# Performance work log

Measured on AMD Instinct MI355X. Metric: run time of the kernel, lower is better.

Reference implementation:

```python
import math
import jax, jax.numpy as jnp
import numpy as np

K = 32        # number of mixtures == feature dim (constructor quirk of GMM)
D = 32        # gaussian feature dim
N = 200_000   # samples


def setup_inputs() -> dict:
    key = jax.random.key(0)
    k1, k2, k3 = jax.random.split(key, 3)
    X = jax.random.normal(k1, (N, D), dtype=jnp.float32)
    # mu initialized as (rand(dims) - 0.5) * 2 per Gaussian
    mus = (jax.random.uniform(k2, (K, D), dtype=jnp.float32) - 0.5) * 2.0
    # SPD covariances near identity (source starts from eye and EM-updates)
    A = jax.random.normal(k3, (K, D, D), dtype=jnp.float32) * 0.1
    sigmas = jnp.eye(D, dtype=jnp.float32)[None] + jnp.einsum('kij,klj->kil', A, A)
    # phi = 1/count_of = 1/dims for every mixture (constructor quirk)
    phis = jnp.full((K,), 1.0 / D, dtype=jnp.float32)
    return {"X": X, "mus": mus, "sigmas": sigmas, "phis": phis}


def reference(X, mus, sigmas, phis):
    # Gaussian.forward (batched over all samples and all mixtures):
    # p_kn = exp(-0.5 * (x_n - mu_k) inv_sigma_k (x_n - mu_k)^T) / sqrt((2pi)^D * det_k)
    d = X.shape[1]
    twopidims = jnp.asarray((2.0 * math.pi) ** d, dtype=X.dtype)
    inv_sigma = jnp.linalg.pinv(sigmas)               # [K,D,D]
    det_sigma = jnp.linalg.det(sigmas)                # [K]
    diff = X[None, :, :] - mus[:, None, :]            # [K,N,D]
    q = jnp.einsum('knd,kde,kne->kn', diff, inv_sigma, diff)  # Mahalanobis [K,N]
    p = jnp.exp(-0.5 * q) / jnp.sqrt(twopidims * det_sigma)[:, None]
    # Mixture.forward with nll=True: -log(phi * p)
    nll = -jnp.log(phis[:, None] * p)                 # [K,N]
    # GMM._probs: stack over mixtures, transpose(0,1), squeeze -> [N,K]
    num = nll.T
    # norm branch: divide each row by its max
    den = jnp.max(num, axis=1, keepdims=True)         # [N,1]
    return num / den
```

## Files before the change

### kernel.cpp

```cpp
#include <hip/hip_runtime.h>

typedef _Float16 f16x8  __attribute__((ext_vector_type(8)));
typedef _Float16 h2v    __attribute__((ext_vector_type(2)));
typedef float    f32x16 __attribute__((ext_vector_type(16)));

#define NSTEP  42
#define NCHUNK 84

__host__ __device__ constexpr int stepDA(int s){
  return s < 4 ? 2*s : s < 12 ? 2*(s-4) : s < 24 ? 2*(s-12) : s < 40 ? 2*(s-24) : -1;
}
__host__ __device__ constexpr int stepDB(int s){
  return s < 40 ? stepDA(s) + 1 : -1;
}
__host__ __device__ constexpr int stepEA(int s){
  return s < 4 ? 0 : s < 12 ? 8 : s < 24 ? 16 : s < 40 ? 24 : (s == 40 ? 0 : 16);
}
__host__ __device__ constexpr int stepEB(int s){
  return s < 40 ? stepEA(s) : (s == 40 ? 8 : 24);
}

__device__ inline float rdlane(float v, int i){
  union { float f; int u; } a, r;
  a.f = v;
  r.u = __builtin_amdgcn_readlane(a.u, i);
  return r.f;
}
__device__ inline unsigned short f2h(float f){
  _Float16 h = (_Float16)f;
  unsigned short u; __builtin_memcpy(&u, &h, 2);
  return u;
}
__device__ inline unsigned pkmulh2(unsigned a, unsigned b){
  h2v x, y; __builtin_memcpy(&x, &a, 4); __builtin_memcpy(&y, &b, 4);
  h2v z = x * y;
  unsigned r; __builtin_memcpy(&r, &z, 4);
  return r;
}

__global__ __launch_bounds__(64) void gmm_prep(
    const float* __restrict__ mus, const float* __restrict__ sigmas,
    const float* __restrict__ phis, unsigned short* __restrict__ Bws,
    float* __restrict__ cstw)
{
  __shared__ float Sld[32 * 33];
  __shared__ float gld[32];

  const int k    = blockIdx.x;
  const int lane = threadIdx.x;
  const int c    = lane & 31;

  float a[32];
  #pragma unroll
  for (int i = 0; i < 32; ++i) a[i] = sigmas[k * 1024 + i * 32 + c];

  float drs = 0.f, dpiv = 1.f;

  #pragma unroll
  for (int j = 0; j < 32; ++j){
    float m    = a[j];
    float d    = rdlane(a[j], j);
    float rs   = rsqrtf(d);
    float rinv = rs * rs;
    if (c == j){ drs = rs; dpiv = d; }
    float mr = m * rinv;
    #pragma unroll
    for (int t = j + 1; t < 32; ++t){
      float s_t = rdlane(a[j], t);
      float upd = a[t] - s_t * mr;
      a[t] = (c > j) ? upd : a[t];
    }
  }

  #pragma unroll
  for (int i = 0; i < 32; ++i) a[i] = (i >= c) ? a[i] * drs : 0.f;

  float r[32];
  #pragma unroll
  for (int i = 0; i < 32; ++i) r[i] = (i == c) ? 1.f : 0.f;
  #pragma unroll
  for (int i = 0; i < 32; ++i){
    float di = rdlane(drs, i);
    float yi = r[i] * di;
    r[i] = yi;
    #pragma unroll
    for (int t = i + 1; t < 32; ++t)
      r[t] -= rdlane(a[t], i) * yi;
  }
  #pragma unroll
  for (int i = 31; i >= 0; --i){
    float di = rdlane(drs, i);
    float xi = r[i] * di;
    r[i] = xi;
    #pragma unroll
    for (int t = 0; t < i; ++t)
      r[t] -= rdlane(a[i], t) * xi;
  }

  float muc = mus[k * 32 + c];
  float g = 0.f;
  #pragma unroll
  for (int i = 0; i < 32; ++i) g += r[i] * rdlane(muc, i);

  float hh = muc * g;
  float ll = logf(dpiv);
  #pragma unroll
  for (int md = 1; md <= 16; md <<= 1){
    hh += __shfl_xor(hh, md);
    ll += __shfl_xor(ll, md);
  }
  if (lane == 0)
    cstw[k] = -logf(phis[k]) + 0.5f * (32.f * 1.8378770664093453f + ll) + 0.5f * hh;

  if (lane < 32){
    #pragma unroll
    for (int i = 0; i < 32; ++i) Sld[i * 33 + c] = r[i];
    gld[c] = g;
  }
  __syncthreads();

  for (int ci = lane; ci < NCHUNK; ci += 64){
    int s2 = ci >> 1, hb = ci & 1;
    int d  = hb ? stepDB(s2) : stepDA(s2);
    int e0 = hb ? stepEB(s2) : stepEA(s2);
    unsigned short u8[8];
    for (int j = 0; j < 8; ++j){
      int e = e0 + j;
      float v;
      if (d < 0)       v = -gld[e];
      else if (e < d)  v = 0.f;
      else if (e == d) v = 0.5f * Sld[d * 33 + d];
      else             v = Sld[d * 33 + e];
      u8[j] = f2h(v);
    }
    uint4 pk; __builtin_memcpy(&pk, u8, 16);
    ((uint4*)Bws)[ci * 32 + k] = pk;
  }
}

__global__ __launch_bounds__(256, 3) void gmm_main(
    const float* __restrict__ X, const unsigned short* __restrict__ Bws,
    const float* __restrict__ cstg, float* __restrict__ out, int N)
{
  __shared__ uint4 ldsB[NSTEP * 64];

  const int tid  = threadIdx.x;
  const int lane = tid & 63;
  const int wv   = tid >> 6;
  const int h    = lane >> 5;
  const int c32  = lane & 31;
  const int blockRow = blockIdx.x * 256;

  const uint4* Bg = (const uint4*)Bws;
  for (int i = tid; i < NSTEP * 64; i += 256) ldsB[i] = Bg[i];

  const unsigned sel = h ? 0x03020302u : 0x01000100u;

  const int r0 = blockRow + wv * 64 + c32;
  const int r1 = r0 + 32;
  const int r0c = r0 < N ? r0 : N - 1;
  const int r1c = r1 < N ? r1 : N - 1;

  unsigned xu0[16], xu1[16];
  {
    const float4* p0 = (const float4*)(X + (size_t)r0c * 32);
    const float4* p1 = (const float4*)(X + (size_t)r1c * 32);
    #pragma unroll
    for (int q = 0; q < 8; ++q){
      float4 v0 = p0[q], v1 = p1[q];
      unsigned short h00 = f2h(v0.x), h01 = f2h(v0.y), h02 = f2h(v0.z), h03 = f2h(v0.w);
      unsigned short h10 = f2h(v1.x), h11 = f2h(v1.y), h12 = f2h(v1.z), h13 = f2h(v1.w);
      xu0[q*2+0] = (unsigned)h00 | ((unsigned)h01 << 16);
      xu0[q*2+1] = (unsigned)h02 | ((unsigned)h03 << 16);
      xu1[q*2+0] = (unsigned)h10 | ((unsigned)h11 << 16);
      xu1[q*2+1] = (unsigned)h12 | ((unsigned)h13 << 16);
    }
  }
  const float cc = cstg[c32];
  __syncthreads();

  f32x16 acc0, acc1;
  #pragma unroll
  for (int i = 0; i < 16; ++i){ acc0[i] = 0.f; acc1[i] = 0.f; }

  union AF { unsigned u[4]; f16x8 v; };
  const f16x8* Bf = (const f16x8*)ldsB;

  #pragma unroll
  for (int s = 0; s < NSTEP; ++s){
    f16x8 bfrag = Bf[(s << 6) + lane];

    AF a0, a1;
    if (s < 40){
      const int p = stepDA(s) >> 1;
      const int e = stepEA(s) >> 1;
      unsigned m0 = __builtin_amdgcn_perm(xu0[p], xu0[p], sel);
      unsigned m1 = __builtin_amdgcn_perm(xu1[p], xu1[p], sel);
      #pragma unroll
      for (int jj = 0; jj < 4; ++jj){
        a0.u[jj] = pkmulh2(m0, xu0[e + jj]);
        a1.u[jj] = pkmulh2(m1, xu1[e + jj]);
      }
    } else {
      const int ea = stepEA(s) >> 1, eb = stepEB(s) >> 1;
      #pragma unroll
      for (int jj = 0; jj < 4; ++jj){
        a0.u[jj] = h ? xu0[eb + jj] : xu0[ea + jj];
        a1.u[jj] = h ? xu1[eb + jj] : xu1[ea + jj];
      }
    }
    acc0 = __builtin_amdgcn_mfma_f32_32x32x16_f16(a0.v, bfrag, acc0, 0, 0, 0);
    acc1 = __builtin_amdgcn_mfma_f32_32x32x16_f16(a1.v, bfrag, acc1, 0, 0, 0);
  }

  #pragma unroll
  for (int rt = 0; rt < 2; ++rt){
    float nll[16], mx[16];
    #pragma unroll
    for (int r = 0; r < 16; ++r){
      float nv = (rt == 0 ? acc0[r] : acc1[r]) + cc;
      nll[r] = nv; mx[r] = nv;
    }
    #pragma unroll
    for (int md = 1; md <= 16; md <<= 1){
      #pragma unroll
      for (int r = 0; r < 16; ++r)
        mx[r] = fmaxf(mx[r], __shfl_xor(mx[r], md));
    }
    const int rowBase = blockRow + wv * 64 + rt * 32;
    #pragma unroll
    for (int r = 0; r < 16; ++r){
      int row = (r & 3) + 8 * (r >> 2) + 4 * h;
      int n = rowBase + row;
      if (n < N) out[(size_t)n * 32 + c32] = nll[r] * __builtin_amdgcn_rcpf(mx[r]);
    }
  }
}

extern "C" void kernel_launch(void* const* d_in, const int* in_sizes, int n_in,
                              void* d_out, int out_size, void* d_ws, size_t ws_size,
                              hipStream_t stream)
{
  const float* X      = (const float*)d_in[0];
  const float* mus    = (const float*)d_in[1];
  const float* sigmas = (const float*)d_in[2];
  const float* phis   = (const float*)d_in[3];
  float* out = (float*)d_out;
  const int N = in_sizes[0] / 32;

  unsigned short* Bws = (unsigned short*)d_ws;
  float* cstw = (float*)((char*)d_ws + NCHUNK * 256 * 2);

  gmm_prep<<<32, 64, 0, stream>>>(mus, sigmas, phis, Bws, cstw);

  const int nb = (N + 255) / 256;
  gmm_main<<<nb, 256, 0, stream>>>(X, Bws, cstw, out, N);
}
```

Measured before the change: 113.9 us.

## Split each wave to one 32-row tile and double waves per block

Each wave now processes a single 32-row MFMA tile instead of two, and the block grows to 512 threads (8 waves) with launch bounds raised to 4 blocks per CU. This halves per-wave register pressure for X fragments and accumulators so more waves can hide MFMA and memory latency. In exchange, each LDS B fragment feeds only one MFMA instead of two, doubling LDS traffic per MFMA. The fp16 conversion of X switches to a packed round-toward-zero convert, slightly changing rounding.

```diff
diff --git a/kernel.cpp b/kernel.cpp
--- a/kernel.cpp
+++ b/kernel.cpp
@@ -3,6 +3,7 @@
 typedef _Float16 f16x8  __attribute__((ext_vector_type(8)));
 typedef _Float16 h2v    __attribute__((ext_vector_type(2)));
 typedef float    f32x16 __attribute__((ext_vector_type(16)));
+typedef unsigned u32x16 __attribute__((ext_vector_type(16)));
 
 #define NSTEP  42
 #define NCHUNK 84
@@ -36,6 +37,11 @@
   h2v z = x * y;
   unsigned r; __builtin_memcpy(&r, &z, 4);
   return r;
+}
+__device__ inline unsigned pkrtz(float lo, float hi){
+  auto p = __builtin_amdgcn_cvt_pkrtz(lo, hi);
+  unsigned u; __builtin_memcpy(&u, &p, 4);
+  return u;
 }
 
 __global__ __launch_bounds__(64) void gmm_prep(
@@ -138,7 +144,44 @@
   }
 }
 
-__global__ __launch_bounds__(256, 3) void gmm_main(
+union AF8 { unsigned u[4]; f16x8 v; };
+
+template<int S>
+__device__ inline void gstep(const f16x8* __restrict__ Bf, int lane, int h,
+                             unsigned sel, const u32x16& xu, f32x16& acc)
+{
+  f16x8 b = Bf[(S << 6) + lane];
+  AF8 a;
+  if constexpr (S < 40){
+    constexpr int p = stepDA(S) >> 1;
+    constexpr int e = stepEA(S) >> 1;
+    unsigned m = __builtin_amdgcn_perm(xu[p], xu[p], sel);
+    a.u[0] = pkmulh2(m, xu[e + 0]);
+    a.u[1] = pkmulh2(m, xu[e + 1]);
+    a.u[2] = pkmulh2(m, xu[e + 2]);
+    a.u[3] = pkmulh2(m, xu[e + 3]);
+  } else {
+    constexpr int ea = stepEA(S) >> 1;
+    constexpr int eb = stepEB(S) >> 1;
+    a.u[0] = h ? xu[eb + 0] : xu[ea + 0];
+    a.u[1] = h ? xu[eb + 1] : xu[ea + 1];
+    a.u[2] = h ? xu[eb + 2] : xu[ea + 2];
+    a.u[3] = h ? xu[eb + 3] : xu[ea + 3];
+  }
+  acc = __builtin_amdgcn_mfma_f32_32x32x16_f16(a.v, b, acc, 0, 0, 0);
+}
+
+template<int S>
+__device__ inline void gsteps(const f16x8* __restrict__ Bf, int lane, int h,
+                              unsigned sel, const u32x16& xu, f32x16& acc)
+{
+  if constexpr (S < NSTEP){
+    gstep<S>(Bf, lane, h, sel, xu, acc);
+    gsteps<S + 1>(Bf, lane, h, sel, xu, acc);
+  }
+}
+
+__global__ __launch_bounds__(512, 4) void gmm_main(
     const float* __restrict__ X, const unsigned short* __restrict__ Bws,
     const float* __restrict__ cstg, float* __restrict__ out, int N)
 {
@@ -152,88 +195,50 @@
   const int blockRow = blockIdx.x * 256;
 
   const uint4* Bg = (const uint4*)Bws;
-  for (int i = tid; i < NSTEP * 64; i += 256) ldsB[i] = Bg[i];
+  for (int i = tid; i < NSTEP * 64; i += 512) ldsB[i] = Bg[i];
 
   const unsigned sel = h ? 0x03020302u : 0x01000100u;
 
-  const int r0 = blockRow + wv * 64 + c32;
-  const int r1 = r0 + 32;
-  const int r0c = r0 < N ? r0 : N - 1;
-  const int r1c = r1 < N ? r1 : N - 1;
-
-  unsigned xu0[16], xu1[16];
+  const int rowi = blockRow + wv * 32 + c32;
+  const int rowc = rowi < N ? rowi : N - 1;
+
+  u32x16 xu;
   {
-    const float4* p0 = (const float4*)(X + (size_t)r0c * 32);
-    const float4* p1 = (const float4*)(X + (size_t)r1c * 32);
+    const float4* xp = (const float4*)(X + (size_t)rowc * 32);
     #pragma unroll
     for (int q = 0; q < 8; ++q){
-      float4 v0 = p0[q], v1 = p1[q];
-      unsigned short h00 = f2h(v0.x), h01 = f2h(v0.y), h02 = f2h(v0.z), h03 = f2h(v0.w);
-      unsigned short h10 = f2h(v1.x), h11 = f2h(v1.y), h12 = f2h(v1.z), h13 = f2h(v1.w);
-      xu0[q*2+0] = (unsigned)h00 | ((unsigned)h01 << 16);
-      xu0[q*2+1] = (unsigned)h02 | ((unsigned)h03 << 16);
-      xu1[q*2+0] = (unsigned)h10 | ((unsigned)h11 << 16);
-      xu1[q*2+1] = (unsigned)h12 | ((unsigned)h13 << 16);
+      float4 v = xp[q];
+      xu[q*2+0] = pkrtz(v.x, v.y);
+      xu[q*2+1] = pkrtz(v.z, v.w);
     }
   }
   const float cc = cstg[c32];
   __syncthreads();
 
-  f32x16 acc0, acc1;
-  #pragma unroll
-  for (int i = 0; i < 16; ++i){ acc0[i] = 0.f; acc1[i] = 0.f; }
-
-  union AF { unsigned u[4]; f16x8 v; };
-  const f16x8* Bf = (const f16x8*)ldsB;
-
-  #pragma unroll
-  for (int s = 0; s < NSTEP; ++s){
-    f16x8 bfrag = Bf[(s << 6) + lane];
-
-    AF a0, a1;
-    if (s < 40){
-      const int p = stepDA(s) >> 1;
-      const int e = stepEA(s) >> 1;
-      unsigned m0 = __builtin_amdgcn_perm(xu0[p], xu0[p], sel);
-      unsigned m1 = __builtin_amdgcn_perm(xu1[p], xu1[p], sel);
-      #pragma unroll
-      for (int jj = 0; jj < 4; ++jj){
-        a0.u[jj] = pkmulh2(m0, xu0[e + jj]);
-        a1.u[jj] = pkmulh2(m1, xu1[e + jj]);
-      }
-    } else {
-      const int ea = stepEA(s) >> 1, eb = stepEB(s) >> 1;
-      #pragma unroll
-      for (int jj = 0; jj < 4; ++jj){
-        a0.u[jj] = h ? xu0[eb + jj] : xu0[ea + jj];
-        a1.u[jj] = h ? xu1[eb + jj] : xu1[ea + jj];
-      }
-    }
-    acc0 = __builtin_amdgcn_mfma_f32_32x32x16_f16(a0.v, bfrag, acc0, 0, 0, 0);
-    acc1 = __builtin_amdgcn_mfma_f32_32x32x16_f16(a1.v, bfrag, acc1, 0, 0, 0);
-  }
-
-  #pragma unroll
-  for (int rt = 0; rt < 2; ++rt){
-    float nll[16], mx[16];
-    #pragma unroll
-    for (int r = 0; r < 16; ++r){
-      float nv = (rt == 0 ? acc0[r] : acc1[r]) + cc;
-      nll[r] = nv; mx[r] = nv;
-    }
-    #pragma unroll
-    for (int md = 1; md <= 16; md <<= 1){
-      #pragma unroll
-      for (int r = 0; r < 16; ++r)
-        mx[r] = fmaxf(mx[r], __shfl_xor(mx[r], md));
-    }
-    const int rowBase = blockRow + wv * 64 + rt * 32;
-    #pragma unroll
-    for (int r = 0; r < 16; ++r){
-      int row = (r & 3) + 8 * (r >> 2) + 4 * h;
-      int n = rowBase + row;
-      if (n < N) out[(size_t)n * 32 + c32] = nll[r] * __builtin_amdgcn_rcpf(mx[r]);
-    }
+  f32x16 acc;
+  #pragma unroll
+  for (int i = 0; i < 16; ++i) acc[i] = 0.f;
+
+  gsteps<0>((const f16x8*)ldsB, lane, h, sel, xu, acc);
+
+  float nll[16], mx[16];
+  #pragma unroll
+  for (int r = 0; r < 16; ++r){
+    float nv = acc[r] + cc;
+    nll[r] = nv; mx[r] = nv;
+  }
+  #pragma unroll
+  for (int md = 1; md <= 16; md <<= 1){
+    #pragma unroll
+    for (int r = 0; r < 16; ++r)
+      mx[r] = fmaxf(mx[r], __shfl_xor(mx[r], md));
+  }
+  const int rowBase = blockRow + wv * 32;
+  #pragma unroll
+  for (int r = 0; r < 16; ++r){
+    int row = (r & 3) + 8 * (r >> 2) + 4 * h;
+    int n = rowBase + row;
+    if (n < N) out[(size_t)n * 32 + c32] = nll[r] * __builtin_amdgcn_rcpf(mx[r]);
   }
 }
 
@@ -254,5 +259,5 @@
   gmm_prep<<<32, 64, 0, stream>>>(mus, sigmas, phis, Bws, cstw);
 
   const int nb = (N + 255) / 256;
-  gmm_main<<<nb, 256, 0, stream>>>(X, Bws, cstw, out, N);
-}
+  gmm_main<<<nb, 512, 0, stream>>>(X, Bws, cstw, out, N);
+}
```

Result: faster. 108.3 us (-4.9%).
